# Performance work log

Hardware: AMD Instinct MI355X
Metric: run time of the kernel (lower is better)

Reference implementation:

```python
import jax, jax.numpy as jnp
import numpy as np

N_NODES = 100000
N_EDGES = 1600000
HIDDEN = 128
N_LAYERS = 3
N_GRAPHS = 100
EPS = 1e-5


def setup_inputs() -> dict:
    key = jax.random.key(0)
    ks = jax.random.split(key, 9)
    node = jax.random.normal(ks[0], (N_NODES, HIDDEN), dtype=jnp.float32)
    edge_index = jax.random.randint(ks[1], (2, N_EDGES), 0, N_NODES, dtype=jnp.int32)
    edge_attr = jax.random.uniform(ks[2], (N_EDGES,), dtype=jnp.float32)
    batch_ptr = jnp.sort(jax.random.randint(ks[3], (N_NODES,), 0, N_GRAPHS, dtype=jnp.int32))
    W = jax.random.normal(ks[4], (N_LAYERS, HIDDEN, HIDDEN), dtype=jnp.float32) * (1.0 / np.sqrt(HIDDEN))
    b = jax.random.normal(ks[5], (N_LAYERS, HIDDEN), dtype=jnp.float32) * 0.02
    gn_weight = jnp.ones((N_LAYERS, HIDDEN), dtype=jnp.float32)
    gn_bias = jnp.zeros((N_LAYERS, HIDDEN), dtype=jnp.float32)
    gn_alpha = jnp.ones((N_LAYERS, HIDDEN), dtype=jnp.float32)
    return {"node": node, "edge_index": edge_index, "edge_attr": edge_attr,
            "batch_ptr": batch_ptr, "W": W, "b": b, "gn_weight": gn_weight,
            "gn_bias": gn_bias, "gn_alpha": gn_alpha}


def reference(node, edge_index, edge_attr, batch_ptr, W, b, gn_weight, gn_bias, gn_alpha):
    N, d = node.shape
    src, dst = edge_index[0], edge_index[1]
    # GCN normalization with self-loops (weight 1), as in PyG gcn_norm
    loop = jnp.arange(N, dtype=src.dtype)
    src_a = jnp.concatenate([src, loop])
    dst_a = jnp.concatenate([dst, loop])
    w_a = jnp.concatenate([edge_attr, jnp.ones((N,), dtype=edge_attr.dtype)])
    deg = jax.ops.segment_sum(w_a, dst_a, num_segments=N)
    dis = jnp.where(deg > 0, deg ** -0.5, 0.0)
    norm = dis[src_a] * w_a * dis[dst_a]  # [E+N]

    counts = jax.ops.segment_sum(jnp.ones((N,), node.dtype), batch_ptr,
                                 num_segments=N_GRAPHS)[:, None]  # [G,1]

    for l in range(W.shape[0]):
        # GCNConv: linear transform, then gather-normalize-scatter over edges
        h = node @ W[l]  # [N,d]
        agg = jax.ops.segment_sum(norm[:, None] * h[src_a], dst_a, num_segments=N) + b[l]
        # GraphNorm: per-graph mean shift (scaled by alpha) and variance norm
        mean = jax.ops.segment_sum(agg, batch_ptr, num_segments=N_GRAPHS) / counts  # [G,d]
        sub = agg - gn_alpha[l] * mean[batch_ptr]
        var = jax.ops.segment_sum(sub * sub, batch_ptr, num_segments=N_GRAPHS) / counts
        node = jax.nn.relu(gn_weight[l] * sub * jax.lax.rsqrt(var[batch_ptr] + EPS) + gn_bias[l])
    return node
```

## Files before the change

kernel.cpp:

```cpp
#include <hip/hip_runtime.h>
#include <cstdint>

#define N_N 100000
#define N_E 1600000
#define HID 128
#define N_G 100
#define EPSF 1e-5f

#define NB   256
#define EPB  ((N_E + NB - 1) / NB)
#define NBKT ((N_N + 255) >> 8)

static inline int ceil_div(int a, int b){ return (a + b - 1) / b; }

typedef __attribute__((ext_vector_type(8))) short bf16x8;
typedef __attribute__((ext_vector_type(4))) float f32x4;

__device__ inline float bf2f(unsigned short u){
  return __uint_as_float(((unsigned int)u) << 16);
}
__device__ inline unsigned short f2bf(float f){
  unsigned int u = __float_as_uint(f);
  unsigned int r = u + 0x7fffu + ((u >> 16) & 1u);
  return (unsigned short)(r >> 16);
}
__device__ inline void fma8(float* acc, float nv, uint4 u){
  acc[0] += nv * __uint_as_float(u.x << 16);
  acc[1] += nv * __uint_as_float(u.x & 0xffff0000u);
  acc[2] += nv * __uint_as_float(u.y << 16);
  acc[3] += nv * __uint_as_float(u.y & 0xffff0000u);
  acc[4] += nv * __uint_as_float(u.z << 16);
  acc[5] += nv * __uint_as_float(u.z & 0xffff0000u);
  acc[6] += nv * __uint_as_float(u.w << 16);
  acc[7] += nv * __uint_as_float(u.w & 0xffff0000u);
}

__global__ void k_wt3(const float* __restrict__ W, unsigned short* __restrict__ Wt,
                      float* __restrict__ counts){
  int i = blockIdx.x * 256 + threadIdx.x;
  if (i < N_G) counts[i] = 0.0f;
  if (i >= 3 * HID * HID) return;
  int l = i >> 14;
  int r = i & 16383;
  int n = r >> 7, k = r & 127;
  Wt[i] = f2bf(W[l * HID * HID + k * HID + n]);
}

__global__ void k_counts(const int* __restrict__ bp, float* __restrict__ counts){
  int t = blockIdx.x * 256 + threadIdx.x;
  int r0 = t * 32;
  if (r0 >= N_N) return;
  int r1 = min(r0 + 32, N_N);
  int curg = bp[r0];
  float acc = 0.f;
  for (int r = r0; r < r1; ++r){
    int g = bp[r];
    if (g != curg){ atomicAdd(&counts[curg], acc); acc = 0.f; curg = g; }
    acc += 1.0f;
  }
  atomicAdd(&counts[curg], acc);
}

__global__ __launch_bounds__(256) void k_hist(const int* __restrict__ dst,
                                              int* __restrict__ counts){
  __shared__ int h[NBKT];
  int t = threadIdx.x, blk = blockIdx.x;
  for (int i = t; i < NBKT; i += 256) h[i] = 0;
  __syncthreads();
  int e0 = blk * EPB, e1 = min(e0 + EPB, N_E);
  for (int e = e0 + t; e < e1; e += 256)
    atomicAdd(&h[dst[e] >> 8], 1);
  __syncthreads();
  for (int i = t; i < NBKT; i += 256) counts[i * NB + blk] = h[i];
}

__global__ __launch_bounds__(256) void k_scanA(int* __restrict__ data,
                                               int* __restrict__ bsum, int n){
  __shared__ int s[256];
  int t = threadIdx.x;
  int i = blockIdx.x * 256 + t;
  int v = (i < n) ? data[i] : 0;
  s[t] = v; __syncthreads();
  #pragma unroll
  for (int off = 1; off < 256; off <<= 1){
    int tmp = (t >= off) ? s[t - off] : 0;
    __syncthreads();
    s[t] += tmp;
    __syncthreads();
  }
  if (i < n) data[i] = s[t] - v;
  if (t == 255) bsum[blockIdx.x] = s[255];
}

__global__ __launch_bounds__(512) void k_scanB(int* __restrict__ bsum, int nblocks){
  __shared__ int s[512];
  int t = threadIdx.x;
  int v = (t < nblocks) ? bsum[t] : 0;
  s[t] = v; __syncthreads();
  #pragma unroll
  for (int off = 1; off < 512; off <<= 1){
    int tmp = (t >= off) ? s[t - off] : 0;
    __syncthreads();
    s[t] += tmp;
    __syncthreads();
  }
  if (t < nblocks) bsum[t] = s[t] - v;
}

__global__ void k_scanC(int* __restrict__ data, const int* __restrict__ bsum, int n){
  int i = blockIdx.x * 256 + threadIdx.x;
  if (i < n) data[i] += bsum[blockIdx.x];
}

__global__ __launch_bounds__(256) void k_part(const int* __restrict__ src,
                                              const int* __restrict__ dst,
                                              const float* __restrict__ w,
                                              const int* __restrict__ coff,
                                              int2* __restrict__ part){
  __shared__ int off[NBKT];
  int t = threadIdx.x, blk = blockIdx.x;
  for (int i = t; i < NBKT; i += 256) off[i] = coff[i * NB + blk];
  __syncthreads();
  int e0 = blk * EPB, e1 = min(e0 + EPB, N_E);
  for (int e = e0 + t; e < e1; e += 256){
    int d = dst[e];
    int pos = atomicAdd(&off[d >> 8], 1);
    part[pos] = make_int2(src[e] | ((d & 255) << 24), __float_as_int(w[e]));
  }
}

__global__ __launch_bounds__(256) void k_csr(const int* __restrict__ coff,
                                             const int2* __restrict__ part,
                                             int2* __restrict__ edge8,
                                             int* __restrict__ ptr,
                                             float* __restrict__ dis,
                                             float* __restrict__ nself){
  __shared__ int h[256];
  __shared__ int c[256];
  __shared__ float wsum[256];
  __shared__ int s[256];
  int t = threadIdx.x, b = blockIdx.x;
  int base  = coff[b * NB];
  int base2 = (b + 1 < NBKT) ? coff[(b + 1) * NB] : N_E;
  h[t] = 0; c[t] = 0; wsum[t] = 0.f;
  __syncthreads();
  for (int e = base + t; e < base2; e += 256){
    int2 v = part[e];
    int local = ((unsigned int)v.x) >> 24;
    atomicAdd(&h[local], 1);
    atomicAdd(&wsum[local], __int_as_float(v.y));
  }
  __syncthreads();
  int v0 = h[t];
  s[t] = v0; __syncthreads();
  #pragma unroll
  for (int off = 1; off < 256; off <<= 1){
    int tmp = (t >= off) ? s[t - off] : 0;
    __syncthreads();
    s[t] += tmp;
    __syncthreads();
  }
  int mybase = base + s[t] - v0;
  int node = (b << 8) + t;
  if (node < N_N){
    ptr[node] = mybase;
    float d = 1.0f + wsum[t];
    float r = rsqrtf(d);
    dis[node] = r;
    nself[node] = r * r;
  }
  if (b == NBKT - 1 && t == 0) ptr[N_N] = N_E;
  h[t] = mybase;
  __syncthreads();
  for (int e = base + t; e < base2; e += 256){
    int2 v = part[e];
    int local = ((unsigned int)v.x) >> 24;
    int pos = h[local] + atomicAdd(&c[local], 1);
    edge8[pos] = make_int2(v.x & 0x00ffffff, v.y);
  }
}

__global__ void k_ne(const int* __restrict__ ptr, const float* __restrict__ dis,
                     int2* __restrict__ edge8){
  int i = blockIdx.x * 256 + threadIdx.x;
  if (i >= N_N) return;
  float di = dis[i];
  int e0 = ptr[i], e1 = ptr[i + 1];
  for (int e = e0; e < e1; ++e){
    int2 v = edge8[e];
    float ne = dis[v.x] * __int_as_float(v.y) * di;
    ((float*)&edge8[e])[1] = ne;
  }
}

__global__ __launch_bounds__(256) void k_gemm(const float* __restrict__ X,
                                              const float* __restrict__ agg,
                                              int fused,
                                              const int* __restrict__ bp,
                                              const float* __restrict__ mean,
                                              const float* __restrict__ rstd,
                                              const float* __restrict__ alpha,
                                              const float* __restrict__ gwv,
                                              const float* __restrict__ gbv,
                                              const unsigned short* __restrict__ Wt,
                                              unsigned short* __restrict__ Hb, int nrows){
  __shared__ unsigned short lA[64 * 136];
  __shared__ unsigned short lB[128 * 136];
  int tid = threadIdx.x;
  int row0 = blockIdx.x * 64;

  #pragma unroll
  for (int i = 0; i < 8; ++i){
    int c = tid + i * 256;
    int r = c >> 4, cc = c & 15;
    *(uint4*)&lB[r * 136 + cc * 8] = ((const uint4*)Wt)[c];
  }
  #pragma unroll
  for (int i = 0; i < 8; ++i){
    int c = tid + i * 256;
    int r = c >> 5, cc = c & 31;
    int gr = row0 + r;
    float4 v = make_float4(0.f, 0.f, 0.f, 0.f);
    if (gr < nrows){
      if (!fused){
        v = *(const float4*)(X + (size_t)gr * HID + cc * 4);
      } else {
        int g = bp[gr];
        float4 a  = *(const float4*)(agg  + (size_t)gr * HID + cc * 4);
        float4 m  = *(const float4*)(mean + g * HID + cc * 4);
        float4 rs = *(const float4*)(rstd + g * HID + cc * 4);
        float4 al = *(const float4*)(alpha + cc * 4);
        float4 wv = *(const float4*)(gwv + cc * 4);
        float4 bv = *(const float4*)(gbv + cc * 4);
        v.x = fmaxf(wv.x * (a.x - al.x * m.x) * rs.x + bv.x, 0.f);
        v.y = fmaxf(wv.y * (a.y - al.y * m.y) * rs.y + bv.y, 0.f);
        v.z = fmaxf(wv.z * (a.z - al.z * m.z) * rs.z + bv.z, 0.f);
        v.w = fmaxf(wv.w * (a.w - al.w * m.w) * rs.w + bv.w, 0.f);
      }
    }
    unsigned short pk[4] = {f2bf(v.x), f2bf(v.y), f2bf(v.z), f2bf(v.w)};
    *(uint2*)&lA[r * 136 + cc * 4] = *(const uint2*)pk;
  }
  __syncthreads();

  int wave = tid >> 6;
  int lane = tid & 63;
  int l16 = lane & 15;
  int quad = lane >> 4;
  int am = wave * 16 + l16;

  bf16x8 afr[4];
  #pragma unroll
  for (int kc = 0; kc < 4; ++kc)
    afr[kc] = *(const bf16x8*)&lA[am * 136 + kc * 32 + quad * 8];

  #pragma unroll
  for (int nt = 0; nt < 8; ++nt){
    f32x4 acc = {0.f, 0.f, 0.f, 0.f};
    int bn = nt * 16 + l16;
    #pragma unroll
    for (int kc = 0; kc < 4; ++kc){
      bf16x8 bfr = *(const bf16x8*)&lB[bn * 136 + kc * 32 + quad * 8];
      acc = __builtin_amdgcn_mfma_f32_16x16x32_bf16(afr[kc], bfr, acc, 0, 0, 0);
    }
    int gr = row0 + wave * 16 + quad * 4;
    #pragma unroll
    for (int r = 0; r < 4; ++r){
      if (gr + r < nrows)
        Hb[(size_t)(gr + r) * HID + nt * 16 + l16] = f2bf(acc[r]);
    }
  }
}

__global__ __launch_bounds__(256) void k_gather(const int* __restrict__ ptr,
                                                const int2* __restrict__ edge8,
                                                const unsigned short* __restrict__ Hb,
                                                const float* __restrict__ nself,
                                                const float* __restrict__ bias,
                                                float* __restrict__ agg){
  int t = blockIdx.x * 256 + threadIdx.x;
  int node = t >> 4;
  if (node >= N_N) return;
  int lane = t & 15;
  const uint4* h16 = (const uint4*)Hb;
  float ns = nself[node];
  uint4 hu = h16[(size_t)node * 16 + lane];
  float4 b0 = ((const float4*)bias)[lane * 2];
  float4 b1 = ((const float4*)bias)[lane * 2 + 1];
  float acc[8] = {b0.x, b0.y, b0.z, b0.w, b1.x, b1.y, b1.z, b1.w};
  fma8(acc, ns, hu);

  int e0 = ptr[node], e1 = ptr[node + 1];
  int e = e0;
  for (; e + 4 <= e1; e += 4){
    int2 ev0 = edge8[e + 0];
    int2 ev1 = edge8[e + 1];
    int2 ev2 = edge8[e + 2];
    int2 ev3 = edge8[e + 3];
    uint4 r0 = h16[(size_t)ev0.x * 16 + lane];
    uint4 r1 = h16[(size_t)ev1.x * 16 + lane];
    uint4 r2 = h16[(size_t)ev2.x * 16 + lane];
    uint4 r3 = h16[(size_t)ev3.x * 16 + lane];
    fma8(acc, __int_as_float(ev0.y), r0);
    fma8(acc, __int_as_float(ev1.y), r1);
    fma8(acc, __int_as_float(ev2.y), r2);
    fma8(acc, __int_as_float(ev3.y), r3);
  }
  for (; e < e1; ++e){
    int2 ev = edge8[e];
    uint4 r0 = h16[(size_t)ev.x * 16 + lane];
    fma8(acc, __int_as_float(ev.y), r0);
  }
  float4* ap = (float4*)(agg + (size_t)node * HID + lane * 8);
  ap[0] = make_float4(acc[0], acc[1], acc[2], acc[3]);
  ap[1] = make_float4(acc[4], acc[5], acc[6], acc[7]);
}


__global__ void k_zero2(float* __restrict__ a, float* __restrict__ b){
  int i = blockIdx.x * 256 + threadIdx.x;
  if (i < N_G * HID){ a[i] = 0.f; b[i] = 0.f; }
}

__global__ __launch_bounds__(128) void k_gstat(const float* __restrict__ agg,
                                               const int* __restrict__ bp,
                                               float* __restrict__ sum,
                                               float* __restrict__ sumsq){
  int f = threadIdx.x;
  int r0 = blockIdx.x * 64;
  int r1 = min(r0 + 64, N_N);
  int curg = bp[r0];
  float s = 0.f, s2 = 0.f;
  for (int r = r0; r < r1; ++r){
    int g = bp[r];
    if (g != curg){
      atomicAdd(&sum[curg * HID + f], s);
      atomicAdd(&sumsq[curg * HID + f], s2);
      s = 0.f; s2 = 0.f; curg = g;
    }
    float v = agg[(size_t)r * HID + f];
    s += v; s2 += v * v;
  }
  atomicAdd(&sum[curg * HID + f], s);
  atomicAdd(&sumsq[curg * HID + f], s2);
}

__global__ void k_finstat(const float* __restrict__ sum, const float* __restrict__ sumsq,
                          const float* __restrict__ counts, const float* __restrict__ alpha,
                          float* __restrict__ mean, float* __restrict__ rstd){
  int i = blockIdx.x * 256 + threadIdx.x;
  if (i >= N_G * HID) return;
  int f = i & (HID - 1);
  float c = counts[i >> 7];
  float inv = c > 0.f ? 1.0f / c : 0.f;
  float m = sum[i] * inv;
  float ex2 = sumsq[i] * inv;
  float al = alpha[f];
  float var = ex2 - m * m * al * (2.0f - al);
  mean[i] = m;
  rstd[i] = rsqrtf(var + EPSF);
}

__global__ void k_out(const float* __restrict__ agg, const int* __restrict__ bp,
                      const float* __restrict__ mean, const float* __restrict__ rstd,
                      const float* __restrict__ alpha, const float* __restrict__ gw,
                      const float* __restrict__ gb, float* __restrict__ out){
  int idx = blockIdx.x * 256 + threadIdx.x;
  if (idx >= N_N * 32) return;
  int i = idx >> 5, q = idx & 31;
  int g = bp[i];
  float4 a  = ((const float4*)agg)[idx];
  float4 m  = ((const float4*)mean)[g * 32 + q];
  float4 r  = ((const float4*)rstd)[g * 32 + q];
  float4 al = ((const float4*)alpha)[q];
  float4 wv = ((const float4*)gw)[q];
  float4 bv = ((const float4*)gb)[q];
  float4 o;
  o.x = fmaxf(wv.x * (a.x - al.x * m.x) * r.x + bv.x, 0.f);
  o.y = fmaxf(wv.y * (a.y - al.y * m.y) * r.y + bv.y, 0.f);
  o.z = fmaxf(wv.z * (a.z - al.z * m.z) * r.z + bv.z, 0.f);
  o.w = fmaxf(wv.w * (a.w - al.w * m.w) * r.w + bv.w, 0.f);
  ((float4*)out)[idx] = o;
}


extern "C" void kernel_launch(void* const* d_in, const int* in_sizes, int n_in,
                              void* d_out, int out_size, void* d_ws, size_t ws_size,
                              hipStream_t stream){
  const float* node0 = (const float*)d_in[0];
  const int*   eidx  = (const int*)d_in[1];
  const float* eattr = (const float*)d_in[2];
  const int*   bp    = (const int*)d_in[3];
  const float* W     = (const float*)d_in[4];
  const float* bias  = (const float*)d_in[5];
  const float* gw    = (const float*)d_in[6];
  const float* gb    = (const float*)d_in[7];
  const float* ga    = (const float*)d_in[8];
  float* out = (float*)d_out;
  const int* src = eidx;
  const int* dst = eidx + N_E;

  char* p = (char*)d_ws;
  auto carve = [&](size_t nbytes) -> char* {
    char* q = p; p += (nbytes + 255) & ~(size_t)255; return q;
  };
  float* dis    = (float*)carve((size_t)N_N * 4);
  float* nself  = (float*)carve((size_t)N_N * 4);
  float* counts = (float*)carve((size_t)N_G * 4);
  int*   coff   = (int*)  carve((size_t)NBKT * NB * 4);
  int*   bsum   = (int*)  carve((size_t)512 * 4);
  int*   ptr    = (int*)  carve((size_t)(N_N + 1) * 4);
  int2*  edge8  = (int2*) carve((size_t)N_E * 8);
  unsigned short* hb = (unsigned short*)carve((size_t)N_N * HID * 2);
  unsigned short* wt = (unsigned short*)carve((size_t)3 * HID * HID * 2);
  float* agg    = (float*)carve((size_t)N_N * HID * 4);
  float* mean   = (float*)carve((size_t)N_G * HID * 4);
  float* rstd   = (float*)carve((size_t)N_G * HID * 4);
  float* sum    = (float*)carve((size_t)N_G * HID * 4);
  float* sumsq  = (float*)carve((size_t)N_G * HID * 4);
  int2*  part   = (int2*)agg;

  int nscan = NBKT * NB;
  int nscan_blocks = ceil_div(nscan, 256);

  k_wt3   <<<ceil_div(3 * HID * HID, 256), 256, 0, stream>>>(W, wt, counts);
  k_counts<<<ceil_div(N_N, 32 * 256), 256, 0, stream>>>(bp, counts);
  k_hist  <<<NB, 256, 0, stream>>>(dst, coff);
  k_scanA <<<nscan_blocks, 256, 0, stream>>>(coff, bsum, nscan);
  k_scanB <<<1, 512, 0, stream>>>(bsum, nscan_blocks);
  k_scanC <<<nscan_blocks, 256, 0, stream>>>(coff, bsum, nscan);
  k_part  <<<NB, 256, 0, stream>>>(src, dst, eattr, coff, part);
  k_csr   <<<NBKT, 256, 0, stream>>>(coff, part, edge8, ptr, dis, nself);
  k_ne    <<<ceil_div(N_N, 256), 256, 0, stream>>>(ptr, dis, edge8);

  for (int l = 0; l < 3; ++l){
    if (l == 0){
      k_gemm <<<ceil_div(N_N, 64), 256, 0, stream>>>(node0, nullptr, 0,
                 nullptr, nullptr, nullptr, nullptr, nullptr, nullptr,
                 wt, hb, N_N);
    } else {
      k_gemm <<<ceil_div(N_N, 64), 256, 0, stream>>>(nullptr, agg, 1,
                 bp, mean, rstd, ga + (l - 1) * HID, gw + (l - 1) * HID,
                 gb + (l - 1) * HID, wt + (size_t)l * HID * HID, hb, N_N);
    }
    if (l == 0){
    }
    k_gather <<<ceil_div(N_N * 16, 256), 256, 0, stream>>>(ptr, edge8, hb, nself,
                 bias + l * HID, agg);
    k_zero2  <<<ceil_div(N_G * HID, 256), 256, 0, stream>>>(sum, sumsq);
    k_gstat  <<<ceil_div(N_N, 64), 128, 0, stream>>>(agg, bp, sum, sumsq);
    k_finstat<<<ceil_div(N_G * HID, 256), 256, 0, stream>>>(sum, sumsq, counts,
                 ga + l * HID, mean, rstd);
  }
  k_out <<<ceil_div(N_N * 32, 256), 256, 0, stream>>>(agg, bp, mean, rstd,
             ga + 2 * HID, gw + 2 * HID, gb + 2 * HID, out);
}
```

Before: 591.9 us.

## Split H into feature slices so gather blocks work on cache-resident column slabs

The GEMM now writes H in eight column-sliced planes of 16 features each, so every slice is a contiguous N x 16 bf16 array. The gather kernel assigns each block one slice and 128 nodes, using two threads per node per slice. The aim is to keep each slice's random-access working set (about 3.2 MB) cache-resident and raise L2 hit rates for the irregular neighbour reads. In exchange, the edge list is read eight times, once per slice, which is why those edge loads and the output stores are marked nontemporal.

```diff
diff --git a/kernel.cpp b/kernel.cpp
--- a/kernel.cpp
+++ b/kernel.cpp
@@ -10,6 +10,9 @@
 #define NB   256
 #define EPB  ((N_E + NB - 1) / NB)
 #define NBKT ((N_N + 255) >> 8)
+
+#define NSL  8
+#define NPB  128
 
 static inline int ceil_div(int a, int b){ return (a + b - 1) / b; }
 
@@ -264,10 +267,11 @@
       acc = __builtin_amdgcn_mfma_f32_16x16x32_bf16(afr[kc], bfr, acc, 0, 0, 0);
     }
     int gr = row0 + wave * 16 + quad * 4;
+    unsigned short* hbs = Hb + (size_t)nt * ((size_t)N_N * 16);
     #pragma unroll
     for (int r = 0; r < 4; ++r){
       if (gr + r < nrows)
-        Hb[(size_t)(gr + r) * HID + nt * 16 + l16] = f2bf(acc[r]);
+        hbs[(size_t)(gr + r) * 16 + l16] = f2bf(acc[r]);
     }
   }
 }
@@ -278,42 +282,45 @@
                                                 const float* __restrict__ nself,
                                                 const float* __restrict__ bias,
                                                 float* __restrict__ agg){
-  int t = blockIdx.x * 256 + threadIdx.x;
-  int node = t >> 4;
+  int s = blockIdx.x & (NSL - 1);
+  int node = (blockIdx.x >> 3) * NPB + (threadIdx.x >> 1);
   if (node >= N_N) return;
-  int lane = t & 15;
-  const uint4* h16 = (const uint4*)Hb;
+  int lane = threadIdx.x & 1;
+  const uint4* hs = (const uint4*)(Hb + (size_t)s * ((size_t)N_N * 16));
   float ns = nself[node];
-  uint4 hu = h16[(size_t)node * 16 + lane];
-  float4 b0 = ((const float4*)bias)[lane * 2];
-  float4 b1 = ((const float4*)bias)[lane * 2 + 1];
+  uint4 hu = hs[(size_t)node * 2 + lane];
+  float4 b0 = ((const float4*)bias)[s * 4 + lane * 2];
+  float4 b1 = ((const float4*)bias)[s * 4 + lane * 2 + 1];
   float acc[8] = {b0.x, b0.y, b0.z, b0.w, b1.x, b1.y, b1.z, b1.w};
   fma8(acc, ns, hu);
 
   int e0 = ptr[node], e1 = ptr[node + 1];
+  const long long* ep = (const long long*)edge8;
   int e = e0;
   for (; e + 4 <= e1; e += 4){
-    int2 ev0 = edge8[e + 0];
-    int2 ev1 = edge8[e + 1];
-    int2 ev2 = edge8[e + 2];
-    int2 ev3 = edge8[e + 3];
-    uint4 r0 = h16[(size_t)ev0.x * 16 + lane];
-    uint4 r1 = h16[(size_t)ev1.x * 16 + lane];
-    uint4 r2 = h16[(size_t)ev2.x * 16 + lane];
-    uint4 r3 = h16[(size_t)ev3.x * 16 + lane];
-    fma8(acc, __int_as_float(ev0.y), r0);
-    fma8(acc, __int_as_float(ev1.y), r1);
-    fma8(acc, __int_as_float(ev2.y), r2);
-    fma8(acc, __int_as_float(ev3.y), r3);
+    long long v0 = __builtin_nontemporal_load(ep + e + 0);
+    long long v1 = __builtin_nontemporal_load(ep + e + 1);
+    long long v2 = __builtin_nontemporal_load(ep + e + 2);
+    long long v3 = __builtin_nontemporal_load(ep + e + 3);
+    uint4 r0 = hs[(size_t)(unsigned int)v0 * 2 + lane];
+    uint4 r1 = hs[(size_t)(unsigned int)v1 * 2 + lane];
+    uint4 r2 = hs[(size_t)(unsigned int)v2 * 2 + lane];
+    uint4 r3 = hs[(size_t)(unsigned int)v3 * 2 + lane];
+    fma8(acc, __uint_as_float((unsigned int)(((unsigned long long)v0) >> 32)), r0);
+    fma8(acc, __uint_as_float((unsigned int)(((unsigned long long)v1) >> 32)), r1);
+    fma8(acc, __uint_as_float((unsigned int)(((unsigned long long)v2) >> 32)), r2);
+    fma8(acc, __uint_as_float((unsigned int)(((unsigned long long)v3) >> 32)), r3);
   }
   for (; e < e1; ++e){
-    int2 ev = edge8[e];
-    uint4 r0 = h16[(size_t)ev.x * 16 + lane];
-    fma8(acc, __int_as_float(ev.y), r0);
-  }
-  float4* ap = (float4*)(agg + (size_t)node * HID + lane * 8);
-  ap[0] = make_float4(acc[0], acc[1], acc[2], acc[3]);
-  ap[1] = make_float4(acc[4], acc[5], acc[6], acc[7]);
+    long long v = __builtin_nontemporal_load(ep + e);
+    uint4 r0 = hs[(size_t)(unsigned int)v * 2 + lane];
+    fma8(acc, __uint_as_float((unsigned int)(((unsigned long long)v) >> 32)), r0);
+  }
+  float* ap = agg + (size_t)node * HID + s * 16 + lane * 8;
+  f32x4 w0 = {acc[0], acc[1], acc[2], acc[3]};
+  f32x4 w1 = {acc[4], acc[5], acc[6], acc[7]};
+  __builtin_nontemporal_store(w0, (f32x4*)ap);
+  __builtin_nontemporal_store(w1, (f32x4*)ap + 1);
 }
 
 
@@ -433,6 +440,8 @@
   k_csr   <<<NBKT, 256, 0, stream>>>(coff, part, edge8, ptr, dis, nself);
   k_ne    <<<ceil_div(N_N, 256), 256, 0, stream>>>(ptr, dis, edge8);
 
+  int gather_blocks = NSL * ceil_div(N_N, NPB);
+
   for (int l = 0; l < 3; ++l){
     if (l == 0){
       k_gemm <<<ceil_div(N_N, 64), 256, 0, stream>>>(node0, nullptr, 0,
@@ -443,9 +452,7 @@
                  bp, mean, rstd, ga + (l - 1) * HID, gw + (l - 1) * HID,
                  gb + (l - 1) * HID, wt + (size_t)l * HID * HID, hb, N_N);
     }
-    if (l == 0){
-    }
-    k_gather <<<ceil_div(N_N * 16, 256), 256, 0, stream>>>(ptr, edge8, hb, nself,
+    k_gather <<<gather_blocks, 256, 0, stream>>>(ptr, edge8, hb, nself,
                  bias + l * HID, agg);
     k_zero2  <<<ceil_div(N_G * HID, 256), 256, 0, stream>>>(sum, sumsq);
     k_gstat  <<<ceil_div(N_N, 64), 128, 0, stream>>>(agg, bp, sum, sumsq);
```

After: 972.1 us. +64.2%, slower.
